# Performance work log

Measured on AMD Instinct MI355X. Metric: run time of the kernel, lower is better.

Reference implementation:

```python
import jax, jax.numpy as jnp
import numpy as np

B, N, S, F = 16, 512, 7, 256
HID, NUM_CLASSES = 1024, 81
FLAT = S * S * F  # 12544


def setup_inputs() -> dict:
    key = jax.random.key(0)
    ks = jax.random.split(key, 8)
    features = jax.random.normal(ks[0], (B, N, S, S, F), dtype=jnp.float32)
    valid_mask = jax.random.randint(ks[1], (B, N), 0, 2) > 0
    W1 = jax.random.normal(ks[2], (FLAT, HID), dtype=jnp.float32) * (1.0 / np.sqrt(FLAT))
    b1 = jnp.zeros((HID,), dtype=jnp.float32)
    W2 = jax.random.normal(ks[3], (HID, HID), dtype=jnp.float32) * (1.0 / np.sqrt(HID))
    b2 = jnp.zeros((HID,), dtype=jnp.float32)
    W3 = jax.random.normal(ks[4], (HID, NUM_CLASSES), dtype=jnp.float32) * (1.0 / np.sqrt(HID))
    b3 = jnp.zeros((NUM_CLASSES,), dtype=jnp.float32)
    return {"features": features, "valid_mask": valid_mask, "W1": W1, "b1": b1,
            "W2": W2, "b2": b2, "W3": W3, "b3": b3, "features_size_pred": N}


def reference(features, valid_mask, W1, b1, W2, b2, W3, b3, features_size_pred):
    # The TF module masks out invalid ROIs, runs the MLP, then scatters results
    # back to original positions (pad + argsort + gather) with zeros for invalid
    # rows. That is mathematically identical to running the MLP on all ROIs and
    # zeroing invalid rows, which is the efficient dense form.
    b, n = features.shape[0], features.shape[1]
    x = features.reshape(b * n, FLAT)                      # [B*N, 12544]
    h = jax.nn.relu(x @ W1 + b1)                           # [B*N, HID]
    h = jax.nn.relu(h @ W2 + b2)                           # [B*N, HID]
    logits = (h @ W3 + b3).reshape(b, n, NUM_CLASSES)      # [B, N, C]
    mask = valid_mask.astype(logits.dtype)[..., None]      # [B, N, 1]
    return logits * mask
```

## Files before the change

### kernel.cpp

```cpp
#include <hip/hip_runtime.h>
#include <stdint.h>

#define DEVINL __device__ __forceinline__

typedef __bf16 bf16x8 __attribute__((ext_vector_type(8)));
typedef float f32x4 __attribute__((ext_vector_type(4)));

DEVINL unsigned short f32_to_bf16(float f) {
  union { float f; uint32_t u; } v;
  v.f = f;
  uint32_t r = v.u + 0x7fffu + ((v.u >> 16) & 1u);
  return (unsigned short)(r >> 16);
}

DEVINL void load16_to_lds(const void* g, void* l) {
  __builtin_amdgcn_global_load_lds(
      (const __attribute__((address_space(1))) void*)g,
      (__attribute__((address_space(3))) void*)l, 16, 0, 0);
}

__global__ __launch_bounds__(1024) void compact_kernel(
    const int* __restrict__ mask, int* __restrict__ ridx, int* __restrict__ nv) {
  __shared__ int tsum[1024];
  __shared__ int wbase[17];
  const int t = threadIdx.x;
  int flags[8];
  int cnt = 0;
#pragma unroll
  for (int i = 0; i < 8; ++i) {
    flags[i] = (mask[t * 8 + i] != 0) ? 1 : 0;
    cnt += flags[i];
  }
  tsum[t] = cnt;
  __syncthreads();
  if ((t & 63) == 0) {
    int s = 0;
    for (int i = 0; i < 64; ++i) { int v = tsum[t + i]; tsum[t + i] = s; s += v; }
    wbase[t >> 6] = s;
  }
  __syncthreads();
  if (t == 0) {
    int s = 0;
    for (int w = 0; w < 16; ++w) { int v = wbase[w]; wbase[w] = s; s += v; }
    wbase[16] = s;
    *nv = s;
  }
  __syncthreads();
  int base = wbase[t >> 6] + tsum[t];
#pragma unroll
  for (int i = 0; i < 8; ++i)
    if (flags[i]) ridx[base++] = t * 8 + i;
  const int Mv = wbase[16];
  const int Mpad = (Mv + 127) & ~127;
  for (int i = Mv + t; i < Mpad; i += 1024) ridx[i] = 0;
}

__global__ __launch_bounds__(256) void zero_out_kernel(float4* __restrict__ o) {
  o[(size_t)blockIdx.x * 256 + threadIdx.x] = float4{0.f, 0.f, 0.f, 0.f};
}

__global__ __launch_bounds__(256) void gather_cast_kernel(
    const float* __restrict__ feat, const int* __restrict__ ridx,
    const int* __restrict__ nv, unsigned short* __restrict__ out) {
  const int Mpad = ((*nv) + 127) & ~127;
  const unsigned idx = blockIdx.x * 256u + threadIdx.x;
  const unsigned crow = idx / 1568u;
  if ((int)crow >= Mpad) return;
  const int off = (int)(idx - crow * 1568u) * 8;
  const float* src = feat + (size_t)ridx[crow] * 12544 + off;
  float4 a = *reinterpret_cast<const float4*>(src);
  float4 b = *reinterpret_cast<const float4*>(src + 4);
  uint4 p;
  p.x = (uint32_t)f32_to_bf16(a.x) | ((uint32_t)f32_to_bf16(a.y) << 16);
  p.y = (uint32_t)f32_to_bf16(a.z) | ((uint32_t)f32_to_bf16(a.w) << 16);
  p.z = (uint32_t)f32_to_bf16(b.x) | ((uint32_t)f32_to_bf16(b.y) << 16);
  p.w = (uint32_t)f32_to_bf16(b.z) | ((uint32_t)f32_to_bf16(b.w) << 16);
  *reinterpret_cast<uint4*>(out + (size_t)crow * 12544 + off) = p;
}

__global__ void transpose_cast_kernel(const float* __restrict__ W,
                                      unsigned short* __restrict__ Wt,
                                      int K, int Nsrc) {
  __shared__ float tile[32][33];
  const int k0 = blockIdx.x * 32;
  const int n0 = blockIdx.y * 32;
  const int t = threadIdx.x;
#pragma unroll
  for (int i = 0; i < 4; ++i) {
    int idx = t + 256 * i;
    int r = idx >> 5, c = idx & 31;
    int gn = n0 + c;
    float v = (gn < Nsrc) ? W[(size_t)(k0 + r) * Nsrc + gn] : 0.0f;
    tile[r][c] = v;
  }
  __syncthreads();
#pragma unroll
  for (int i = 0; i < 4; ++i) {
    int idx = t + 256 * i;
    int n = idx >> 5, k = idx & 31;
    Wt[(size_t)(n0 + n) * K + (k0 + k)] = f32_to_bf16(tile[k][n]);
  }
}

template <int BM, int BN, bool A_F32, bool RELU_BF16_OUT>
__global__ __launch_bounds__(256) void gemm_kernel(
    const void* __restrict__ Ap, const unsigned short* __restrict__ Bt,
    const float* __restrict__ bias, unsigned short* __restrict__ Hout,
    float* __restrict__ Fout, const int* __restrict__ ridx,
    const int* __restrict__ nv, int K, int Nout, int ldo) {
  constexpr int WM = BM / 32;
  constexpr int WN = BN / 32;
  const int Mv = *nv;
  const int Mpad = (Mv + 127) & ~127;
  const int m0 = blockIdx.y * BM;
  if (m0 >= Mpad) return;

  __shared__ alignas(16) unsigned short Asmem[BM * 32];
  __shared__ alignas(16) unsigned short Bsmem[BN * 32];

  const int tid = threadIdx.x;
  const int wave = tid >> 6, lane = tid & 63;
  const int wm = wave >> 1, wn = wave & 1;
  const int n0 = blockIdx.x * BN;

  const float* Af = (const float*)Ap;
  const unsigned short* Ab = (const unsigned short*)Ap;

  f32x4 acc[WM][WN] = {};

  for (int k0 = 0; k0 < K; k0 += 32) {
    if constexpr (A_F32) {
      constexpr int NF4 = (BM * 32) / (256 * 4);
#pragma unroll
      for (int i = 0; i < NF4; ++i) {
        int idx = tid + 256 * i;
        int r = idx >> 3, c4 = idx & 7;
        float4 v = *reinterpret_cast<const float4*>(
            Af + (size_t)ridx[m0 + r] * K + (k0 + c4 * 4));
        uint2 p;
        p.x = (uint32_t)f32_to_bf16(v.x) | ((uint32_t)f32_to_bf16(v.y) << 16);
        p.y = (uint32_t)f32_to_bf16(v.z) | ((uint32_t)f32_to_bf16(v.w) << 16);
        *reinterpret_cast<uint2*>(&Asmem[r * 32 + c4 * 4]) = p;
      }
    } else {
#pragma unroll
      for (int c = wave; c < BM / 16; c += 4) {
        int row = c * 16 + (lane >> 2);
        load16_to_lds(Ab + (size_t)(m0 + row) * K + (k0 + (lane & 3) * 8),
                      &Asmem[c * 512]);
      }
    }
#pragma unroll
    for (int c = wave; c < BN / 16; c += 4) {
      int row = c * 16 + (lane >> 2);
      load16_to_lds(Bt + (size_t)(n0 + row) * K + (k0 + (lane & 3) * 8),
                    &Bsmem[c * 512]);
    }
    __syncthreads();

    bf16x8 a[WM], b[WN];
#pragma unroll
    for (int i = 0; i < WM; ++i)
      a[i] = *reinterpret_cast<const bf16x8*>(
          &Asmem[(wm * WM * 16 + i * 16 + (lane & 15)) * 32 + (lane >> 4) * 8]);
#pragma unroll
    for (int j = 0; j < WN; ++j)
      b[j] = *reinterpret_cast<const bf16x8*>(
          &Bsmem[(wn * WN * 16 + j * 16 + (lane & 15)) * 32 + (lane >> 4) * 8]);
#pragma unroll
    for (int i = 0; i < WM; ++i)
#pragma unroll
      for (int j = 0; j < WN; ++j)
        acc[i][j] = __builtin_amdgcn_mfma_f32_16x16x32_bf16(a[i], b[j],
                                                            acc[i][j], 0, 0, 0);
    __syncthreads();
  }

  const int l15 = lane & 15, quad = lane >> 4;
#pragma unroll
  for (int j = 0; j < WN; ++j) {
    int n = n0 + wn * WN * 16 + j * 16 + l15;
    if (n >= Nout) continue;
    float bn = bias[n];
#pragma unroll
    for (int i = 0; i < WM; ++i) {
      int mb = m0 + wm * WM * 16 + i * 16 + quad * 4;
      f32x4 v = acc[i][j];
#pragma unroll
      for (int r = 0; r < 4; ++r) {
        int m = mb + r;
        if constexpr (RELU_BF16_OUT) {
          Hout[(size_t)m * ldo + n] = f32_to_bf16(fmaxf(v[r] + bn, 0.0f));
        } else {
          if (m < Mv) Fout[(size_t)ridx[m] * ldo + n] = v[r] + bn;
        }
      }
    }
  }
}

extern "C" void kernel_launch(void* const* d_in, const int* in_sizes, int n_in,
                              void* d_out, int out_size, void* d_ws,
                              size_t ws_size, hipStream_t stream) {
  const float* feat = (const float*)d_in[0];
  const int* mask = (const int*)d_in[1];
  const float* W1 = (const float*)d_in[2];
  const float* b1 = (const float*)d_in[3];
  const float* W2 = (const float*)d_in[4];
  const float* b2 = (const float*)d_in[5];
  const float* W3 = (const float*)d_in[6];
  const float* b3 = (const float*)d_in[7];
  float* out = (float*)d_out;

  char* ws = (char*)d_ws;
  size_t off = 0;
  int* ridx = (int*)(ws + off); off += 32768;
  int* nv   = (int*)(ws + off); off += 256;
  unsigned short* W1t = (unsigned short*)(ws + off); off += 25690112;
  unsigned short* W2t = (unsigned short*)(ws + off); off += 2097152;
  unsigned short* W3t = (unsigned short*)(ws + off); off += 196608;
  unsigned short* H1  = (unsigned short*)(ws + off); off += 16777216;
  unsigned short* H2  = (unsigned short*)(ws + off); off += 16777216;
  unsigned short* Fb  = (unsigned short*)(ws + off);
  size_t need = off + 205520896;

  compact_kernel<<<1, 1024, 0, stream>>>(mask, ridx, nv);
  zero_out_kernel<<<648, 256, 0, stream>>>((float4*)out);
  transpose_cast_kernel<<<dim3(392, 32), 256, 0, stream>>>(W1, W1t, 12544, 1024);
  transpose_cast_kernel<<<dim3(32, 32), 256, 0, stream>>>(W2, W2t, 1024, 1024);
  transpose_cast_kernel<<<dim3(32, 3), 256, 0, stream>>>(W3, W3t, 1024, 81);

  if (ws_size >= need) {
    gather_cast_kernel<<<50176, 256, 0, stream>>>(feat, ridx, nv, Fb);
    gemm_kernel<128, 128, false, true><<<dim3(8, 64), 256, 0, stream>>>(
        Fb, W1t, b1, H1, nullptr, ridx, nv, 12544, 1024, 1024);
  } else {
    gemm_kernel<128, 128, true, true><<<dim3(8, 64), 256, 0, stream>>>(
        feat, W1t, b1, H1, nullptr, ridx, nv, 12544, 1024, 1024);
  }
  gemm_kernel<128, 128, false, true><<<dim3(8, 64), 256, 0, stream>>>(
      H1, W2t, b2, H2, nullptr, ridx, nv, 1024, 1024, 1024);
  gemm_kernel<32, 96, false, false><<<dim3(1, 256), 256, 0, stream>>>(
      H2, W3t, b3, nullptr, out, ridx, nv, 1024, 81, 81);
}
```

Baseline: 964.0 us.

## Split-K the first GEMM with reduce kernel and double-buffer LDS tiles

The large first GEMM (K=12544) is split four ways along K, giving four times as many workgroups. Each split writes fp32 partial sums to a workspace buffer, and a new reduce kernel adds them, applies bias and ReLU, and casts to bf16. All GEMMs also switch to double-buffered LDS, so the loads for the next K tile are issued before the MFMAs on the current one. This costs extra global traffic for the fp32 partials (about 128MB), one more kernel launch, and twice the LDS per block.

```diff
diff --git a/kernel.cpp b/kernel.cpp
--- a/kernel.cpp
+++ b/kernel.cpp
@@ -102,12 +102,35 @@
   }
 }
 
-template <int BM, int BN, bool A_F32, bool RELU_BF16_OUT>
+__global__ __launch_bounds__(256) void reduce_relu_kernel(
+    const float* __restrict__ P, const float* __restrict__ bias,
+    const int* __restrict__ nv, unsigned short* __restrict__ H) {
+  const int Mpad = ((*nv) + 127) & ~127;
+  const int m = blockIdx.x;
+  if (m >= Mpad) return;
+  const int n = threadIdx.x * 4;
+  f32x4 s = {};
+#pragma unroll
+  for (int c = 0; c < 4; ++c) {
+    f32x4 v = *reinterpret_cast<const f32x4*>(
+        P + ((size_t)c * 8192 + m) * 1024 + n);
+    s[0] += v[0]; s[1] += v[1]; s[2] += v[2]; s[3] += v[3];
+  }
+  f32x4 bv = *reinterpret_cast<const f32x4*>(bias + n);
+  uint2 o;
+  o.x = (uint32_t)f32_to_bf16(fmaxf(s[0] + bv[0], 0.0f)) |
+        ((uint32_t)f32_to_bf16(fmaxf(s[1] + bv[1], 0.0f)) << 16);
+  o.y = (uint32_t)f32_to_bf16(fmaxf(s[2] + bv[2], 0.0f)) |
+        ((uint32_t)f32_to_bf16(fmaxf(s[3] + bv[3], 0.0f)) << 16);
+  *reinterpret_cast<uint2*>(H + (size_t)m * 1024 + n) = o;
+}
+
+template <int BM, int BN, bool A_F32, int OMODE>
 __global__ __launch_bounds__(256) void gemm_kernel(
     const void* __restrict__ Ap, const unsigned short* __restrict__ Bt,
     const float* __restrict__ bias, unsigned short* __restrict__ Hout,
     float* __restrict__ Fout, const int* __restrict__ ridx,
-    const int* __restrict__ nv, int K, int Nout, int ldo) {
+    const int* __restrict__ nv, int K, int k_len, int Nout, int ldo) {
   constexpr int WM = BM / 32;
   constexpr int WN = BN / 32;
   const int Mv = *nv;
@@ -115,20 +138,22 @@
   const int m0 = blockIdx.y * BM;
   if (m0 >= Mpad) return;
 
-  __shared__ alignas(16) unsigned short Asmem[BM * 32];
-  __shared__ alignas(16) unsigned short Bsmem[BN * 32];
+  __shared__ alignas(16) unsigned short As[2][BM * 32];
+  __shared__ alignas(16) unsigned short Bs[2][BN * 32];
 
   const int tid = threadIdx.x;
   const int wave = tid >> 6, lane = tid & 63;
   const int wm = wave >> 1, wn = wave & 1;
   const int n0 = blockIdx.x * BN;
+  const int ks = blockIdx.z * k_len;
+  const int ke = ks + k_len;
 
   const float* Af = (const float*)Ap;
   const unsigned short* Ab = (const unsigned short*)Ap;
 
   f32x4 acc[WM][WN] = {};
 
-  for (int k0 = 0; k0 < K; k0 += 32) {
+  auto stage = [&](int b, int k0) {
     if constexpr (A_F32) {
       constexpr int NF4 = (BM * 32) / (256 * 4);
 #pragma unroll
@@ -140,48 +165,59 @@
         uint2 p;
         p.x = (uint32_t)f32_to_bf16(v.x) | ((uint32_t)f32_to_bf16(v.y) << 16);
         p.y = (uint32_t)f32_to_bf16(v.z) | ((uint32_t)f32_to_bf16(v.w) << 16);
-        *reinterpret_cast<uint2*>(&Asmem[r * 32 + c4 * 4]) = p;
+        *reinterpret_cast<uint2*>(&As[b][r * 32 + c4 * 4]) = p;
       }
     } else {
 #pragma unroll
       for (int c = wave; c < BM / 16; c += 4) {
         int row = c * 16 + (lane >> 2);
         load16_to_lds(Ab + (size_t)(m0 + row) * K + (k0 + (lane & 3) * 8),
-                      &Asmem[c * 512]);
+                      &As[b][c * 512]);
       }
     }
 #pragma unroll
     for (int c = wave; c < BN / 16; c += 4) {
       int row = c * 16 + (lane >> 2);
       load16_to_lds(Bt + (size_t)(n0 + row) * K + (k0 + (lane & 3) * 8),
-                    &Bsmem[c * 512]);
+                    &Bs[b][c * 512]);
     }
-    __syncthreads();
-
-    bf16x8 a[WM], b[WN];
+  };
+
+  auto compute = [&](int b) {
+    bf16x8 a[WM], bb[WN];
 #pragma unroll
     for (int i = 0; i < WM; ++i)
       a[i] = *reinterpret_cast<const bf16x8*>(
-          &Asmem[(wm * WM * 16 + i * 16 + (lane & 15)) * 32 + (lane >> 4) * 8]);
+          &As[b][(wm * WM * 16 + i * 16 + (lane & 15)) * 32 + (lane >> 4) * 8]);
 #pragma unroll
     for (int j = 0; j < WN; ++j)
-      b[j] = *reinterpret_cast<const bf16x8*>(
-          &Bsmem[(wn * WN * 16 + j * 16 + (lane & 15)) * 32 + (lane >> 4) * 8]);
+      bb[j] = *reinterpret_cast<const bf16x8*>(
+          &Bs[b][(wn * WN * 16 + j * 16 + (lane & 15)) * 32 + (lane >> 4) * 8]);
 #pragma unroll
     for (int i = 0; i < WM; ++i)
 #pragma unroll
       for (int j = 0; j < WN; ++j)
-        acc[i][j] = __builtin_amdgcn_mfma_f32_16x16x32_bf16(a[i], b[j],
+        acc[i][j] = __builtin_amdgcn_mfma_f32_16x16x32_bf16(a[i], bb[j],
                                                             acc[i][j], 0, 0, 0);
+  };
+
+  stage(0, ks);
+  __syncthreads();
+  int cur = 0;
+  for (int k0 = ks + 32; k0 < ke; k0 += 32) {
+    stage(cur ^ 1, k0);
+    compute(cur);
     __syncthreads();
-  }
+    cur ^= 1;
+  }
+  compute(cur);
 
   const int l15 = lane & 15, quad = lane >> 4;
 #pragma unroll
   for (int j = 0; j < WN; ++j) {
     int n = n0 + wn * WN * 16 + j * 16 + l15;
     if (n >= Nout) continue;
-    float bn = bias[n];
+    float bn = (OMODE == 2) ? 0.0f : bias[n];
 #pragma unroll
     for (int i = 0; i < WM; ++i) {
       int mb = m0 + wm * WM * 16 + i * 16 + quad * 4;
@@ -189,10 +225,12 @@
 #pragma unroll
       for (int r = 0; r < 4; ++r) {
         int m = mb + r;
-        if constexpr (RELU_BF16_OUT) {
+        if constexpr (OMODE == 0) {
           Hout[(size_t)m * ldo + n] = f32_to_bf16(fmaxf(v[r] + bn, 0.0f));
+        } else if constexpr (OMODE == 1) {
+          if (m < Mv) Fout[(size_t)ridx[m] * ldo + n] = v[r] + bn;
         } else {
-          if (m < Mv) Fout[(size_t)ridx[m] * ldo + n] = v[r] + bn;
+          Fout[((size_t)blockIdx.z * 8192 + m) * (size_t)ldo + n] = v[r];
         }
       }
     }
@@ -221,8 +259,10 @@
   unsigned short* W3t = (unsigned short*)(ws + off); off += 196608;
   unsigned short* H1  = (unsigned short*)(ws + off); off += 16777216;
   unsigned short* H2  = (unsigned short*)(ws + off); off += 16777216;
-  unsigned short* Fb  = (unsigned short*)(ws + off);
-  size_t need = off + 205520896;
+  unsigned short* Fb  = (unsigned short*)(ws + off); off += 205520896;
+  size_t need_base = off;
+  float* P = (float*)(ws + off); off += 134217728;
+  size_t need_split = off;
 
   compact_kernel<<<1, 1024, 0, stream>>>(mask, ridx, nv);
   zero_out_kernel<<<648, 256, 0, stream>>>((float4*)out);
@@ -230,16 +270,21 @@
   transpose_cast_kernel<<<dim3(32, 32), 256, 0, stream>>>(W2, W2t, 1024, 1024);
   transpose_cast_kernel<<<dim3(32, 3), 256, 0, stream>>>(W3, W3t, 1024, 81);
 
-  if (ws_size >= need) {
+  if (ws_size >= need_split) {
     gather_cast_kernel<<<50176, 256, 0, stream>>>(feat, ridx, nv, Fb);
-    gemm_kernel<128, 128, false, true><<<dim3(8, 64), 256, 0, stream>>>(
-        Fb, W1t, b1, H1, nullptr, ridx, nv, 12544, 1024, 1024);
+    gemm_kernel<128, 128, false, 2><<<dim3(8, 64, 4), 256, 0, stream>>>(
+        Fb, W1t, b1, nullptr, P, ridx, nv, 12544, 3136, 1024, 1024);
+    reduce_relu_kernel<<<8192, 256, 0, stream>>>(P, b1, nv, H1);
+  } else if (ws_size >= need_base) {
+    gather_cast_kernel<<<50176, 256, 0, stream>>>(feat, ridx, nv, Fb);
+    gemm_kernel<128, 128, false, 0><<<dim3(8, 64, 1), 256, 0, stream>>>(
+        Fb, W1t, b1, H1, nullptr, ridx, nv, 12544, 12544, 1024, 1024);
   } else {
-    gemm_kernel<128, 128, true, true><<<dim3(8, 64), 256, 0, stream>>>(
-        feat, W1t, b1, H1, nullptr, ridx, nv, 12544, 1024, 1024);
-  }
-  gemm_kernel<128, 128, false, true><<<dim3(8, 64), 256, 0, stream>>>(
-      H1, W2t, b2, H2, nullptr, ridx, nv, 1024, 1024, 1024);
-  gemm_kernel<32, 96, false, false><<<dim3(1, 256), 256, 0, stream>>>(
-      H2, W3t, b3, nullptr, out, ridx, nv, 1024, 81, 81);
-}
+    gemm_kernel<128, 128, true, 0><<<dim3(8, 64, 1), 256, 0, stream>>>(
+        feat, W1t, b1, H1, nullptr, ridx, nv, 12544, 12544, 1024, 1024);
+  }
+  gemm_kernel<128, 128, false, 0><<<dim3(8, 64, 1), 256, 0, stream>>>(
+      H1, W2t, b2, H2, nullptr, ridx, nv, 1024, 1024, 1024, 1024);
+  gemm_kernel<32, 96, false, 1><<<dim3(1, 256, 1), 256, 0, stream>>>(
+      H2, W3t, b3, nullptr, out, ridx, nv, 1024, 1024, 81, 81);
+}
```

Measured after the change: 836.5 us. 13.2% less time.
